# Kernel optimization log

Measured on AMD Instinct MI355X. Metric: run time of the kernel, lower is better.

## Reference

```python
import jax, jax.numpy as jnp
import numpy as np

B, T, D = 4096, 200, 64
NEG_INF = jnp.float32(-2**32 + 1)


def setup_inputs() -> dict:
    key = jax.random.key(0)
    ks = jax.random.split(key, 8)
    queries = jax.random.normal(ks[0], (B, 1, D), dtype=jnp.float32)
    keys = jax.random.normal(ks[1], (B, T, D), dtype=jnp.float32)
    key_masks = jax.random.randint(ks[2], (B, 1, T), 0, 2) > 0
    W1 = jax.random.normal(ks[3], (4 * D, 8), dtype=jnp.float32) * 0.1
    b1 = jnp.zeros((8,), dtype=jnp.float32)
    W2 = jax.random.normal(ks[4], (8, 4), dtype=jnp.float32) * 0.1
    b2 = jnp.zeros((4,), dtype=jnp.float32)
    W3 = jax.random.normal(ks[5], (4, 1), dtype=jnp.float32) * 0.1
    b3 = jnp.zeros((1,), dtype=jnp.float32)
    return {"queries": queries, "keys": keys, "key_masks": key_masks,
            "W1": W1, "b1": b1, "W2": W2, "b2": b2, "W3": W3, "b3": b3}


def reference(queries, keys, key_masks, W1, b1, W2, b2, W3, b3):
    # queries: [B,1,D] -> broadcast to [B,T,D] (repeat_elements)
    q = jnp.broadcast_to(queries, keys.shape)
    # att_input: [B,T,4D]
    att_in = jnp.concatenate([q, keys, q - keys, q * keys], axis=-1)
    h = jax.nn.sigmoid(att_in @ W1 + b1)   # [B,T,8]
    h = jax.nn.sigmoid(h @ W2 + b2)        # [B,T,4]
    score = h @ W3 + b3                    # [B,T,1]
    scores = jnp.transpose(score, (0, 2, 1))  # [B,1,T]
    scores = jnp.where(key_masks, scores, NEG_INF)
    attn = jax.nn.softmax(scores, axis=-1)    # weight_normalization=True
    return attn @ keys                        # [B,1,D]
```

## Files before the change

### kernel.cpp

```cpp
#include <hip/hip_runtime.h>

#define TT 200
#define DD 64
#define BLOCK 256
#define KSH 68
#define CWS 132

typedef unsigned short u16;
typedef unsigned int u32;
typedef __attribute__((ext_vector_type(8))) short short8v;
typedef __attribute__((ext_vector_type(4))) float f32x4;

union Frag { uint2 h[2]; short8v v; };

__device__ __forceinline__ float bflo(u32 w) {
    union { u32 u; float f; } v; v.u = w << 16; return v.f;
}
__device__ __forceinline__ float bfhi(u32 w) {
    union { u32 u; float f; } v; v.u = w & 0xFFFF0000u; return v.f;
}
__device__ __forceinline__ u16 f2bf(float f) {
    union { float f; u32 u; } v; v.f = f;
    return (u16)((v.u + 0x7FFFu + ((v.u >> 16) & 1u)) >> 16);
}
__device__ __forceinline__ u32 cvt_pk_bf16(float lo, float hi) {
    u32 r;
    asm("v_cvt_pk_bf16_f32 %0, %1, %2" : "=v"(r) : "v"(lo), "v"(hi));
    return r;
}
__device__ __forceinline__ float sigmoid_fast(float x) {
    return __builtin_amdgcn_rcpf(1.0f + __expf(-x));
}

#define BARRIER() do {                                              \
    asm volatile("s_waitcnt lgkmcnt(0)" ::: "memory");              \
    __builtin_amdgcn_sched_barrier(0);                              \
    __builtin_amdgcn_s_barrier();                                   \
    __builtin_amdgcn_sched_barrier(0);                              \
} while (0)

__global__ __launch_bounds__(BLOCK, 4) void attn_pool_kernel(
    const float* __restrict__ queries, const float* __restrict__ keys,
    const int* __restrict__ masks, const float* __restrict__ W1,
    const float* __restrict__ b1, const float* __restrict__ W2,
    const float* __restrict__ b2, const float* __restrict__ W3,
    const float* __restrict__ b3, float* __restrict__ out)
{
    __shared__ __align__(16) u16   lds_kh[TT][KSH];
    __shared__ __align__(16) u16   lds_cwt[16][CWS];
    __shared__ __align__(16) u16   lds_q16[DD];
    __shared__ __align__(16) float lds_s[TT][8];
    __shared__ __align__(16) float lds_w[52];
    __shared__ __align__(16) float lds_e[TT];
    __shared__ __align__(16) float red[4];
    float* part = (float*)&lds_s[0][0];

    const int b = blockIdx.x;
    const int tid = threadIdx.x;
    const int wave = tid >> 6;
    const int lane = tid & 63;

    const float4* kp = (const float4*)(keys + (size_t)b * TT * DD);
    float4 L0[4], L1[4], L2[4], L3;
#pragma unroll
    for (int j = 0; j < 4; ++j) L0[j] = kp[(j << 8) + tid];
#pragma unroll
    for (int j = 0; j < 4; ++j) L1[j] = kp[1024 + (j << 8) + tid];
    __builtin_amdgcn_sched_barrier(0);

    int m0 = 0, m1 = 0;
    if (tid < 100) {
        m0 = masks[(size_t)b * TT + tid];
        m1 = masks[(size_t)b * TT + tid + 100];
    }
    const int d_f = tid & 63;
    const int jr = tid >> 6;
    const float w1c0 = W1[(128 + d_f) * 8 + jr];
    const float wbc0 = W1[(64 + d_f) * 8 + jr] - w1c0;
    const float wd0  = W1[(192 + d_f) * 8 + jr];
    const float wac0 = W1[d_f * 8 + jr] + w1c0;
    const float w1c1 = W1[(128 + d_f) * 8 + jr + 4];
    const float wbc1 = W1[(64 + d_f) * 8 + jr + 4] - w1c1;
    const float wd1  = W1[(192 + d_f) * 8 + jr + 4];
    const float wac1 = W1[d_f * 8 + jr + 4] + w1c1;
    const float qd   = queries[(size_t)b * DD + d_f];
    float wv = 0.0f;
    if (tid < 32)       wv = W2[tid];
    else if (tid < 36)  wv = W3[tid - 32];
    else if (tid < 40)  wv = b2[tid - 36];
    else if (tid < 48)  wv = b1[tid - 40];
    else if (tid == 48) wv = b3[0];
    __builtin_amdgcn_sched_barrier(0);

#pragma unroll
    for (int j = 0; j < 4; ++j) {
        int idx = (j << 8) + tid;
        float4 v = L0[j];
        uint2 wp; wp.x = cvt_pk_bf16(v.x, v.y); wp.y = cvt_pk_bf16(v.z, v.w);
        *(uint2*)&lds_kh[idx >> 4][(idx & 15) << 2] = wp;
    }
#pragma unroll
    for (int j = 0; j < 4; ++j) L2[j] = kp[2048 + (j << 8) + tid];
    L3 = kp[3072 + (tid & 127)];
    __builtin_amdgcn_sched_barrier(0);

    lds_cwt[jr][64 + d_f]     = f2bf(wac0);
    lds_cwt[jr + 4][64 + d_f] = f2bf(wac1);
    lds_cwt[jr][d_f]          = f2bf(fmaf(qd, wd0, wbc0));
    lds_cwt[jr + 4][d_f]      = f2bf(fmaf(qd, wd1, wbc1));
    if (tid < DD) lds_q16[tid] = f2bf(qd);
    if (tid < 49) lds_w[tid] = wv;
    BARRIER();

    const int r = lane & 15, g = lane >> 4;
    Frag bf0, bf1, bq0, bq1, aq0, aq1;
    bf0.h[0] = *(const uint2*)&lds_cwt[r][g * 8];
    bf0.h[1] = *(const uint2*)&lds_cwt[r][g * 8 + 4];
    bf1.h[0] = *(const uint2*)&lds_cwt[r][32 + g * 8];
    bf1.h[1] = *(const uint2*)&lds_cwt[r][32 + g * 8 + 4];
    bq0.h[0] = *(const uint2*)&lds_cwt[r][64 + g * 8];
    bq0.h[1] = *(const uint2*)&lds_cwt[r][64 + g * 8 + 4];
    bq1.h[0] = *(const uint2*)&lds_cwt[r][96 + g * 8];
    bq1.h[1] = *(const uint2*)&lds_cwt[r][96 + g * 8 + 4];
    aq0.h[0] = *(const uint2*)&lds_q16[g * 8];
    aq0.h[1] = *(const uint2*)&lds_q16[g * 8 + 4];
    aq1.h[0] = *(const uint2*)&lds_q16[32 + g * 8];
    aq1.h[1] = *(const uint2*)&lds_q16[32 + g * 8 + 4];
    f32x4 zero = {0.0f, 0.0f, 0.0f, 0.0f};
    f32x4 acc_base = __builtin_amdgcn_mfma_f32_16x16x32_bf16(aq1.v, bq1.v, zero, 0, 0, 0);
    acc_base = __builtin_amdgcn_mfma_f32_16x16x32_bf16(aq0.v, bq0.v, acc_base, 0, 0, 0);

    auto gemm_tile = [&](int t0) {
        Frag a0, a1;
        a0.h[0] = *(const uint2*)&lds_kh[t0 + r][g * 8];
        a0.h[1] = *(const uint2*)&lds_kh[t0 + r][g * 8 + 4];
        a1.h[0] = *(const uint2*)&lds_kh[t0 + r][32 + g * 8];
        a1.h[1] = *(const uint2*)&lds_kh[t0 + r][32 + g * 8 + 4];
        f32x4 acc = __builtin_amdgcn_mfma_f32_16x16x32_bf16(a0.v, bf0.v, acc_base, 0, 0, 0);
        acc = __builtin_amdgcn_mfma_f32_16x16x32_bf16(a1.v, bf1.v, acc, 0, 0, 0);
        if (r < 8) {
            const int rr = t0 + (g << 2);
            lds_s[rr + 0][r] = acc[0];
            lds_s[rr + 1][r] = acc[1];
            lds_s[rr + 2][r] = acc[2];
            lds_s[rr + 3][r] = acc[3];
        }
    };
    auto stage4 = [&](const float4* Lv, int base) {
#pragma unroll
        for (int j = 0; j < 4; ++j) {
            int idx = base + (j << 8) + tid;
            float4 v = Lv[j];
            uint2 wp; wp.x = cvt_pk_bf16(v.x, v.y); wp.y = cvt_pk_bf16(v.z, v.w);
            *(uint2*)&lds_kh[idx >> 4][(idx & 15) << 2] = wp;
        }
    };

    gemm_tile(wave << 4);
    stage4(L1, 1024);
    BARRIER();
    gemm_tile((4 + wave) << 4);
    stage4(L2, 2048);
    BARRIER();
    gemm_tile((8 + wave) << 4);
    if (tid < 128) {
        int idx = 3072 + tid;
        float4 v = L3;
        uint2 wp; wp.x = cvt_pk_bf16(v.x, v.y); wp.y = cvt_pk_bf16(v.z, v.w);
        *(uint2*)&lds_kh[idx >> 4][(idx & 15) << 2] = wp;
    }
    BARRIER();
    if (wave == 0) gemm_tile(TT - 16);
    BARRIER();

    float epart = 0.0f;
    if (tid < 100) {
        const int t0 = tid, t1 = tid + 100;
        float4 sa0 = *(const float4*)&lds_s[t0][0];
        float4 sa1 = *(const float4*)&lds_s[t0][4];
        float4 sb0 = *(const float4*)&lds_s[t1][0];
        float4 sb1 = *(const float4*)&lds_s[t1][4];
        float4 b1A = *(const float4*)&lds_w[40];
        float4 b1B = *(const float4*)&lds_w[44];
        float h1a[8], h1b[8];
        h1a[0] = sigmoid_fast(sa0.x + b1A.x); h1b[0] = sigmoid_fast(sb0.x + b1A.x);
        h1a[1] = sigmoid_fast(sa0.y + b1A.y); h1b[1] = sigmoid_fast(sb0.y + b1A.y);
        h1a[2] = sigmoid_fast(sa0.z + b1A.z); h1b[2] = sigmoid_fast(sb0.z + b1A.z);
        h1a[3] = sigmoid_fast(sa0.w + b1A.w); h1b[3] = sigmoid_fast(sb0.w + b1A.w);
        h1a[4] = sigmoid_fast(sa1.x + b1B.x); h1b[4] = sigmoid_fast(sb1.x + b1B.x);
        h1a[5] = sigmoid_fast(sa1.y + b1B.y); h1b[5] = sigmoid_fast(sb1.y + b1B.y);
        h1a[6] = sigmoid_fast(sa1.z + b1B.z); h1b[6] = sigmoid_fast(sb1.z + b1B.z);
        h1a[7] = sigmoid_fast(sa1.w + b1B.w); h1b[7] = sigmoid_fast(sb1.w + b1B.w);
        float sa = lds_w[48], sb = lds_w[48];
#pragma unroll
        for (int c = 0; c < 4; ++c) {
            float ha = lds_w[36 + c], hb = ha;
#pragma unroll
            for (int j = 0; j < 8; ++j) {
                float w2 = lds_w[j * 4 + c];
                ha = fmaf(h1a[j], w2, ha);
                hb = fmaf(h1b[j], w2, hb);
            }
            float w3 = lds_w[32 + c];
            sa = fmaf(sigmoid_fast(ha), w3, sa);
            sb = fmaf(sigmoid_fast(hb), w3, sb);
        }
        float ea = m0 ? __expf(sa) : 0.0f;
        float eb = m1 ? __expf(sb) : 0.0f;
        lds_e[t0] = ea;
        lds_e[t1] = eb;
        epart = ea + eb;
    }
#pragma unroll
    for (int off = 32; off; off >>= 1) epart += __shfl_xor(epart, off, 64);
    if (lane == 0) red[wave] = epart;
    BARRIER();

    {
        const int half = lane >> 5;
        const int dp = lane & 31;
        const int d0 = dp << 1;
        const int tbase = (wave << 1) + half;
        float acc0 = 0.0f, acc1 = 0.0f;
#pragma unroll
        for (int i = 0; i < 25; ++i) {
            const int t = tbase + (i << 3);
            u32 kw = *(const u32*)&lds_kh[t][d0];
            float e = lds_e[t];
            acc0 = fmaf(e, bflo(kw), acc0);
            acc1 = fmaf(e, bfhi(kw), acc1);
        }
        acc0 += __shfl_xor(acc0, 32, 64);
        acc1 += __shfl_xor(acc1, 32, 64);
        if (half == 0) {
            float2 wpack; wpack.x = acc0; wpack.y = acc1;
            *(float2*)&part[wave * DD + d0] = wpack;
        }
    }
    BARRIER();

    if (wave == 0) {
        float tot = red[0] + red[1] + red[2] + red[3];
        float rr = part[lane] + part[DD + lane] + part[2 * DD + lane] + part[3 * DD + lane];
        out[(size_t)b * DD + lane] = rr / tot;
    }
}

extern "C" void kernel_launch(void* const* d_in, const int* in_sizes, int n_in,
                              void* d_out, int out_size, void* d_ws, size_t ws_size,
                              hipStream_t stream) {
    const float* queries = (const float*)d_in[0];
    const float* keys    = (const float*)d_in[1];
    const int*   masks   = (const int*)d_in[2];
    const float* W1      = (const float*)d_in[3];
    const float* b1      = (const float*)d_in[4];
    const float* W2      = (const float*)d_in[5];
    const float* b2      = (const float*)d_in[6];
    const float* W3      = (const float*)d_in[7];
    const float* b3      = (const float*)d_in[8];
    float* out = (float*)d_out;

    const int B = in_sizes[0] / DD;
    attn_pool_kernel<<<B, BLOCK, 0, stream>>>(queries, keys, masks, W1, b1, W2, b2, W3, b3, out);
}
```

Measured before the change: 38.69 us.

## Drop one block barrier and spread MLP epilogue across 200 threads

The last staging of bf16 keys (chunks 2 and 3) is merged before a single barrier, so the third GEMM tile runs after it and one block-wide barrier is removed. The per-timestep MLP/exp epilogue now uses 200 threads with one timestep each instead of 100 threads with two, which shortens the serial dependency chain per thread. Mask loading is adjusted to one element per thread to match. The trade-off is less overlap between the third tile's MFMA and the final staging writes.

```diff
diff --git a/kernel.cpp b/kernel.cpp
--- a/kernel.cpp
+++ b/kernel.cpp
@@ -61,18 +61,15 @@
     const int lane = tid & 63;
 
     const float4* kp = (const float4*)(keys + (size_t)b * TT * DD);
-    float4 L0[4], L1[4], L2[4], L3;
+    float4 L0[4], L1[4], L2[4], L2x;
 #pragma unroll
     for (int j = 0; j < 4; ++j) L0[j] = kp[(j << 8) + tid];
 #pragma unroll
     for (int j = 0; j < 4; ++j) L1[j] = kp[1024 + (j << 8) + tid];
     __builtin_amdgcn_sched_barrier(0);
 
-    int m0 = 0, m1 = 0;
-    if (tid < 100) {
-        m0 = masks[(size_t)b * TT + tid];
-        m1 = masks[(size_t)b * TT + tid + 100];
-    }
+    int msk = 0;
+    if (tid < TT) msk = masks[(size_t)b * TT + tid];
     const int d_f = tid & 63;
     const int jr = tid >> 6;
     const float w1c0 = W1[(128 + d_f) * 8 + jr];
@@ -101,7 +98,7 @@
     }
 #pragma unroll
     for (int j = 0; j < 4; ++j) L2[j] = kp[2048 + (j << 8) + tid];
-    L3 = kp[3072 + (tid & 127)];
+    L2x = kp[3072 + (tid & 127)];
     __builtin_amdgcn_sched_barrier(0);
 
     lds_cwt[jr][64 + d_f]     = f2bf(wac0);
@@ -146,70 +143,62 @@
             lds_s[rr + 3][r] = acc[3];
         }
     };
-    auto stage4 = [&](const float4* Lv, int base) {
-#pragma unroll
-        for (int j = 0; j < 4; ++j) {
-            int idx = base + (j << 8) + tid;
-            float4 v = Lv[j];
-            uint2 wp; wp.x = cvt_pk_bf16(v.x, v.y); wp.y = cvt_pk_bf16(v.z, v.w);
-            *(uint2*)&lds_kh[idx >> 4][(idx & 15) << 2] = wp;
-        }
-    };
 
     gemm_tile(wave << 4);
-    stage4(L1, 1024);
+#pragma unroll
+    for (int j = 0; j < 4; ++j) {
+        int idx = 1024 + (j << 8) + tid;
+        float4 v = L1[j];
+        uint2 wp; wp.x = cvt_pk_bf16(v.x, v.y); wp.y = cvt_pk_bf16(v.z, v.w);
+        *(uint2*)&lds_kh[idx >> 4][(idx & 15) << 2] = wp;
+    }
     BARRIER();
     gemm_tile((4 + wave) << 4);
-    stage4(L2, 2048);
-    BARRIER();
-    gemm_tile((8 + wave) << 4);
+#pragma unroll
+    for (int j = 0; j < 4; ++j) {
+        int idx = 2048 + (j << 8) + tid;
+        float4 v = L2[j];
+        uint2 wp; wp.x = cvt_pk_bf16(v.x, v.y); wp.y = cvt_pk_bf16(v.z, v.w);
+        *(uint2*)&lds_kh[idx >> 4][(idx & 15) << 2] = wp;
+    }
     if (tid < 128) {
         int idx = 3072 + tid;
-        float4 v = L3;
-        uint2 wp; wp.x = cvt_pk_bf16(v.x, v.y); wp.y = cvt_pk_bf16(v.z, v.w);
-        *(uint2*)&lds_kh[idx >> 4][(idx & 15) << 2] = wp;
-    }
-    BARRIER();
+        float4 v = L2x;
+        uint2 wp; wp.x = cvt_pk_bf16(v.x, v.y); wp.y = cvt_pk_bf16(v.z, v.w);
+        *(uint2*)&lds_kh[idx >> 4][(idx & 15) << 2] = wp;
+    }
+    BARRIER();
+    gemm_tile((8 + wave) << 4);
     if (wave == 0) gemm_tile(TT - 16);
     BARRIER();
 
     float epart = 0.0f;
-    if (tid < 100) {
-        const int t0 = tid, t1 = tid + 100;
-        float4 sa0 = *(const float4*)&lds_s[t0][0];
-        float4 sa1 = *(const float4*)&lds_s[t0][4];
-        float4 sb0 = *(const float4*)&lds_s[t1][0];
-        float4 sb1 = *(const float4*)&lds_s[t1][4];
+    if (tid < TT) {
+        float4 s0 = *(const float4*)&lds_s[tid][0];
+        float4 s1 = *(const float4*)&lds_s[tid][4];
         float4 b1A = *(const float4*)&lds_w[40];
         float4 b1B = *(const float4*)&lds_w[44];
-        float h1a[8], h1b[8];
-        h1a[0] = sigmoid_fast(sa0.x + b1A.x); h1b[0] = sigmoid_fast(sb0.x + b1A.x);
-        h1a[1] = sigmoid_fast(sa0.y + b1A.y); h1b[1] = sigmoid_fast(sb0.y + b1A.y);
-        h1a[2] = sigmoid_fast(sa0.z + b1A.z); h1b[2] = sigmoid_fast(sb0.z + b1A.z);
-        h1a[3] = sigmoid_fast(sa0.w + b1A.w); h1b[3] = sigmoid_fast(sb0.w + b1A.w);
-        h1a[4] = sigmoid_fast(sa1.x + b1B.x); h1b[4] = sigmoid_fast(sb1.x + b1B.x);
-        h1a[5] = sigmoid_fast(sa1.y + b1B.y); h1b[5] = sigmoid_fast(sb1.y + b1B.y);
-        h1a[6] = sigmoid_fast(sa1.z + b1B.z); h1b[6] = sigmoid_fast(sb1.z + b1B.z);
-        h1a[7] = sigmoid_fast(sa1.w + b1B.w); h1b[7] = sigmoid_fast(sb1.w + b1B.w);
-        float sa = lds_w[48], sb = lds_w[48];
+        float h1[8];
+        h1[0] = sigmoid_fast(s0.x + b1A.x);
+        h1[1] = sigmoid_fast(s0.y + b1A.y);
+        h1[2] = sigmoid_fast(s0.z + b1A.z);
+        h1[3] = sigmoid_fast(s0.w + b1A.w);
+        h1[4] = sigmoid_fast(s1.x + b1B.x);
+        h1[5] = sigmoid_fast(s1.y + b1B.y);
+        h1[6] = sigmoid_fast(s1.z + b1B.z);
+        h1[7] = sigmoid_fast(s1.w + b1B.w);
+        float sc = lds_w[48];
 #pragma unroll
         for (int c = 0; c < 4; ++c) {
-            float ha = lds_w[36 + c], hb = ha;
-#pragma unroll
-            for (int j = 0; j < 8; ++j) {
-                float w2 = lds_w[j * 4 + c];
-                ha = fmaf(h1a[j], w2, ha);
-                hb = fmaf(h1b[j], w2, hb);
-            }
-            float w3 = lds_w[32 + c];
-            sa = fmaf(sigmoid_fast(ha), w3, sa);
-            sb = fmaf(sigmoid_fast(hb), w3, sb);
-        }
-        float ea = m0 ? __expf(sa) : 0.0f;
-        float eb = m1 ? __expf(sb) : 0.0f;
-        lds_e[t0] = ea;
-        lds_e[t1] = eb;
-        epart = ea + eb;
+            float h = lds_w[36 + c];
+#pragma unroll
+            for (int j = 0; j < 8; ++j)
+                h = fmaf(h1[j], lds_w[j * 4 + c], h);
+            sc = fmaf(sigmoid_fast(h), lds_w[32 + c], sc);
+        }
+        float e = msk ? __expf(sc) : 0.0f;
+        lds_e[tid] = e;
+        epart = e;
     }
 #pragma unroll
     for (int off = 32; off; off >>= 1) epart += __shfl_xor(epart, off, 64);
```

Result: slower. 40.18 us (+3.9%).

## Shrink LDS footprint to fit five blocks per CU

Applied to the files above, without the earlier changes.

Cuts shared memory by storing first-layer scores as bf16, halving the weight tile to 8 rows, and aliasing the softmax and reduction buffers onto the weight tile. Small MLP weights are now read straight from global memory (uniform loads) instead of being staged in LDS. Launch bounds go from 4 to 5 blocks per CU, aiming for more concurrent blocks to hide memory latency. The trade-offs are some precision loss from bf16 rounding of the scores and more register pressure under the tighter launch bound.

```diff
diff --git a/kernel.cpp b/kernel.cpp
--- a/kernel.cpp
+++ b/kernel.cpp
@@ -8,6 +8,7 @@
 
 typedef unsigned short u16;
 typedef unsigned int u32;
+typedef __attribute__((ext_vector_type(8))) u16 ushort8;
 typedef __attribute__((ext_vector_type(8))) short short8v;
 typedef __attribute__((ext_vector_type(4))) float f32x4;
 
@@ -18,6 +19,9 @@
 }
 __device__ __forceinline__ float bfhi(u32 w) {
     union { u32 u; float f; } v; v.u = w & 0xFFFF0000u; return v.f;
+}
+__device__ __forceinline__ float bf2f(u16 h) {
+    union { u32 u; float f; } v; v.u = ((u32)h) << 16; return v.f;
 }
 __device__ __forceinline__ u16 f2bf(float f) {
     union { float f; u32 u; } v; v.f = f;
@@ -39,21 +43,20 @@
     __builtin_amdgcn_sched_barrier(0);                              \
 } while (0)
 
-__global__ __launch_bounds__(BLOCK, 4) void attn_pool_kernel(
+__global__ __launch_bounds__(BLOCK, 5) void attn_pool_kernel(
     const float* __restrict__ queries, const float* __restrict__ keys,
     const int* __restrict__ masks, const float* __restrict__ W1,
     const float* __restrict__ b1, const float* __restrict__ W2,
     const float* __restrict__ b2, const float* __restrict__ W3,
     const float* __restrict__ b3, float* __restrict__ out)
 {
-    __shared__ __align__(16) u16   lds_kh[TT][KSH];
-    __shared__ __align__(16) u16   lds_cwt[16][CWS];
-    __shared__ __align__(16) u16   lds_q16[DD];
-    __shared__ __align__(16) float lds_s[TT][8];
-    __shared__ __align__(16) float lds_w[52];
-    __shared__ __align__(16) float lds_e[TT];
-    __shared__ __align__(16) float red[4];
-    float* part = (float*)&lds_s[0][0];
+    __shared__ __align__(16) u16 lds_kh[TT][KSH];
+    __shared__ __align__(16) u16 lds_cwt[8][CWS];
+    __shared__ __align__(16) u16 lds_q16[DD];
+    __shared__ __align__(16) u16 lds_s[TT][8];
+    float* lds_e = (float*)&lds_cwt[0][0];
+    float* red   = lds_e + TT;
+    float* part  = (float*)&lds_s[0][0];
 
     const int b = blockIdx.x;
     const int tid = threadIdx.x;
@@ -84,12 +87,6 @@
     const float wd1  = W1[(192 + d_f) * 8 + jr + 4];
     const float wac1 = W1[d_f * 8 + jr + 4] + w1c1;
     const float qd   = queries[(size_t)b * DD + d_f];
-    float wv = 0.0f;
-    if (tid < 32)       wv = W2[tid];
-    else if (tid < 36)  wv = W3[tid - 32];
-    else if (tid < 40)  wv = b2[tid - 36];
-    else if (tid < 48)  wv = b1[tid - 40];
-    else if (tid == 48) wv = b3[0];
     __builtin_amdgcn_sched_barrier(0);
 
 #pragma unroll
@@ -109,19 +106,19 @@
     lds_cwt[jr][d_f]          = f2bf(fmaf(qd, wd0, wbc0));
     lds_cwt[jr + 4][d_f]      = f2bf(fmaf(qd, wd1, wbc1));
     if (tid < DD) lds_q16[tid] = f2bf(qd);
-    if (tid < 49) lds_w[tid] = wv;
     BARRIER();
 
     const int r = lane & 15, g = lane >> 4;
+    const int r7 = r & 7;
     Frag bf0, bf1, bq0, bq1, aq0, aq1;
-    bf0.h[0] = *(const uint2*)&lds_cwt[r][g * 8];
-    bf0.h[1] = *(const uint2*)&lds_cwt[r][g * 8 + 4];
-    bf1.h[0] = *(const uint2*)&lds_cwt[r][32 + g * 8];
-    bf1.h[1] = *(const uint2*)&lds_cwt[r][32 + g * 8 + 4];
-    bq0.h[0] = *(const uint2*)&lds_cwt[r][64 + g * 8];
-    bq0.h[1] = *(const uint2*)&lds_cwt[r][64 + g * 8 + 4];
-    bq1.h[0] = *(const uint2*)&lds_cwt[r][96 + g * 8];
-    bq1.h[1] = *(const uint2*)&lds_cwt[r][96 + g * 8 + 4];
+    bf0.h[0] = *(const uint2*)&lds_cwt[r7][g * 8];
+    bf0.h[1] = *(const uint2*)&lds_cwt[r7][g * 8 + 4];
+    bf1.h[0] = *(const uint2*)&lds_cwt[r7][32 + g * 8];
+    bf1.h[1] = *(const uint2*)&lds_cwt[r7][32 + g * 8 + 4];
+    bq0.h[0] = *(const uint2*)&lds_cwt[r7][64 + g * 8];
+    bq0.h[1] = *(const uint2*)&lds_cwt[r7][64 + g * 8 + 4];
+    bq1.h[0] = *(const uint2*)&lds_cwt[r7][96 + g * 8];
+    bq1.h[1] = *(const uint2*)&lds_cwt[r7][96 + g * 8 + 4];
     aq0.h[0] = *(const uint2*)&lds_q16[g * 8];
     aq0.h[1] = *(const uint2*)&lds_q16[g * 8 + 4];
     aq1.h[0] = *(const uint2*)&lds_q16[32 + g * 8];
@@ -140,10 +137,10 @@
         acc = __builtin_amdgcn_mfma_f32_16x16x32_bf16(a1.v, bf1.v, acc, 0, 0, 0);
         if (r < 8) {
             const int rr = t0 + (g << 2);
-            lds_s[rr + 0][r] = acc[0];
-            lds_s[rr + 1][r] = acc[1];
-            lds_s[rr + 2][r] = acc[2];
-            lds_s[rr + 3][r] = acc[3];
+            lds_s[rr + 0][r] = f2bf(acc[0]);
+            lds_s[rr + 1][r] = f2bf(acc[1]);
+            lds_s[rr + 2][r] = f2bf(acc[2]);
+            lds_s[rr + 3][r] = f2bf(acc[3]);
         }
     };
     auto stage4 = [&](const float4* Lv, int base) {
@@ -176,32 +173,26 @@
     float epart = 0.0f;
     if (tid < 100) {
         const int t0 = tid, t1 = tid + 100;
-        float4 sa0 = *(const float4*)&lds_s[t0][0];
-        float4 sa1 = *(const float4*)&lds_s[t0][4];
-        float4 sb0 = *(const float4*)&lds_s[t1][0];
-        float4 sb1 = *(const float4*)&lds_s[t1][4];
-        float4 b1A = *(const float4*)&lds_w[40];
-        float4 b1B = *(const float4*)&lds_w[44];
+        ushort8 sa8 = *(const ushort8*)&lds_s[t0][0];
+        ushort8 sb8 = *(const ushort8*)&lds_s[t1][0];
         float h1a[8], h1b[8];
-        h1a[0] = sigmoid_fast(sa0.x + b1A.x); h1b[0] = sigmoid_fast(sb0.x + b1A.x);
-        h1a[1] = sigmoid_fast(sa0.y + b1A.y); h1b[1] = sigmoid_fast(sb0.y + b1A.y);
-        h1a[2] = sigmoid_fast(sa0.z + b1A.z); h1b[2] = sigmoid_fast(sb0.z + b1A.z);
-        h1a[3] = sigmoid_fast(sa0.w + b1A.w); h1b[3] = sigmoid_fast(sb0.w + b1A.w);
-        h1a[4] = sigmoid_fast(sa1.x + b1B.x); h1b[4] = sigmoid_fast(sb1.x + b1B.x);
-        h1a[5] = sigmoid_fast(sa1.y + b1B.y); h1b[5] = sigmoid_fast(sb1.y + b1B.y);
-        h1a[6] = sigmoid_fast(sa1.z + b1B.z); h1b[6] = sigmoid_fast(sb1.z + b1B.z);
-        h1a[7] = sigmoid_fast(sa1.w + b1B.w); h1b[7] = sigmoid_fast(sb1.w + b1B.w);
-        float sa = lds_w[48], sb = lds_w[48];
+#pragma unroll
+        for (int j = 0; j < 8; ++j) {
+            float bj = b1[j];
+            h1a[j] = sigmoid_fast(bf2f(sa8[j]) + bj);
+            h1b[j] = sigmoid_fast(bf2f(sb8[j]) + bj);
+        }
+        float sa = b3[0], sb = b3[0];
 #pragma unroll
         for (int c = 0; c < 4; ++c) {
-            float ha = lds_w[36 + c], hb = ha;
+            float ha = b2[c], hb = ha;
 #pragma unroll
             for (int j = 0; j < 8; ++j) {
-                float w2 = lds_w[j * 4 + c];
+                float w2 = W2[j * 4 + c];
                 ha = fmaf(h1a[j], w2, ha);
                 hb = fmaf(h1b[j], w2, hb);
             }
-            float w3 = lds_w[32 + c];
+            float w3 = W3[c];
             sa = fmaf(sigmoid_fast(ha), w3, sa);
             sb = fmaf(sigmoid_fast(hb), w3, sb);
         }
```

After: 38.45 us. About the same (-0.6%).
